# Kernel optimization log

Measured on AMD Instinct MI355X. Metric: run time of the kernel, lower is better.

The kernel has to match this reference:

```python
import jax, jax.numpy as jnp
import numpy as np
from jax import lax

NUM_CLASSES = 80
BOX_GAIN, CLS_GAIN, OBJ_GAIN = 7.5, 0.5, 1.0
LABEL_SMOOTH = 0.0
BATCH, NUM_T, IMG = 16, 256, 640
EPS = 1e-7


def setup_inputs() -> dict:
    key = jax.random.key(0)
    ks = jax.random.split(key, 10)
    inp = {}
    for i, g in enumerate([80, 40, 20]):
        inp[f"cls_p{i}"] = jax.random.normal(ks[i], (BATCH, NUM_CLASSES, g, g), jnp.float32)
        inp[f"reg_p{i}"] = jax.random.normal(ks[3 + i], (BATCH, 4, g, g), jnp.float32) * 0.5
    cxy = jax.random.uniform(ks[6], (NUM_T, 2), minval=32.0, maxval=float(IMG - 32))
    wh = jax.random.uniform(ks[7], (NUM_T, 2), minval=8.0, maxval=128.0)
    inp["tboxes"] = jnp.concatenate([cxy - wh / 2, cxy + wh / 2], axis=-1)  # [T,4] xyxy px
    inp["t_batch"] = jax.random.randint(ks[8], (NUM_T,), 0, BATCH, jnp.int32)
    inp["t_cls"] = jax.random.randint(ks[9], (NUM_T,), 0, NUM_CLASSES, jnp.int32)
    return inp


def _bce(z, t):
    # BCEWithLogits: softplus(z) - z*t, numerically stable
    return jnp.logaddexp(0.0, z) - z * t


def _box_iou(a, b):
    # a: [B,A,4] xyxy, b: [T,4] xyxy -> [B,A,T]
    lt = jnp.maximum(a[:, :, None, :2], b[None, None, :, :2])
    rb = jnp.minimum(a[:, :, None, 2:], b[None, None, :, 2:])
    wh = jnp.clip(rb - lt, 0.0)
    inter = wh[..., 0] * wh[..., 1]
    area_a = (a[..., 2] - a[..., 0]) * (a[..., 3] - a[..., 1])
    area_b = (b[:, 2] - b[:, 0]) * (b[:, 3] - b[:, 1])
    return inter / (area_a[:, :, None] + area_b[None, None, :] - inter + EPS)


def _ciou(p, g):
    # elementwise CIoU between matched boxes, p/g: [B,A,4] xyxy -> [B,A]
    pw, ph = p[..., 2] - p[..., 0], p[..., 3] - p[..., 1]
    gw, gh = g[..., 2] - g[..., 0], g[..., 3] - g[..., 1]
    lt = jnp.maximum(p[..., :2], g[..., :2])
    rb = jnp.minimum(p[..., 2:], g[..., 2:])
    wh = jnp.clip(rb - lt, 0.0)
    inter = wh[..., 0] * wh[..., 1]
    union = pw * ph + gw * gh - inter + EPS
    iou = inter / union
    clt = jnp.minimum(p[..., :2], g[..., :2])
    crb = jnp.maximum(p[..., 2:], g[..., 2:])
    c = crb - clt
    c2 = c[..., 0] ** 2 + c[..., 1] ** 2 + EPS  # enclosing diag^2
    pc = (p[..., :2] + p[..., 2:]) * 0.5
    gc = (g[..., :2] + g[..., 2:]) * 0.5
    rho2 = jnp.sum((pc - gc) ** 2, axis=-1)  # center dist^2
    v = (4.0 / jnp.pi ** 2) * (jnp.arctan(gw / (gh + EPS)) - jnp.arctan(pw / (ph + EPS))) ** 2
    alpha = lax.stop_gradient(v / (v - iou + 1.0 + EPS))
    return iou - rho2 / c2 - alpha * v


def _scale_loss(cls_p, reg_p, tboxes, t_batch, t_cls, stride):
    B, C, H, W = cls_p.shape
    A = H * W
    cls_p = cls_p.reshape(B, C, A).transpose(0, 2, 1)  # [B,A,C]
    reg_p = reg_p.reshape(B, 4, A).transpose(0, 2, 1)  # [B,A,4]
    gy, gx = jnp.meshgrid(jnp.arange(H, dtype=jnp.float32), jnp.arange(W, dtype=jnp.float32), indexing="ij")
    grid = jnp.stack([gx, gy], axis=-1).reshape(A, 2)  # [A,2] (x,y), row-major over (h,w)
    # decode: xy = (sigmoid + grid)*stride, wh = exp*stride -> xyxy
    xy = (jax.nn.sigmoid(reg_p[..., :2]) + grid) * stride
    wh = jnp.exp(reg_p[..., 2:4]) * stride
    boxes = jnp.concatenate([xy - wh * 0.5, xy + wh * 0.5], axis=-1)  # [B,A,4]
    # pairwise IoU vs all targets, mask targets from other images
    iou = _box_iou(boxes, tboxes)  # [B,A,T]
    valid = t_batch[None, None, :] == jnp.arange(B, dtype=t_batch.dtype)[:, None, None]
    iou = jnp.where(valid, iou, -1.0)
    max_iou = jnp.max(iou, axis=-1)
    best = jnp.argmax(iou, axis=-1)  # [B,A]
    pos = max_iou > 0.5  # positive anchor mask
    npos = jnp.maximum(jnp.sum(pos), 1)
    # box loss: (1 - CIoU) averaged over positives
    mt_boxes = tboxes[best]  # [B,A,4] gathered matched GT
    ciou = _ciou(boxes, mt_boxes)
    box_loss = jnp.sum(jnp.where(pos, 1.0 - ciou, 0.0)) / npos
    # cls loss: BCE with (smoothed) one-hot over positive anchors
    cp, cn = 1.0 - 0.5 * LABEL_SMOOTH, 0.5 * LABEL_SMOOTH
    cls_t = jax.nn.one_hot(t_cls[best], C, dtype=cls_p.dtype) * (cp - cn) + cn
    cls_loss = jnp.sum(_bce(cls_p, cls_t) * pos[..., None]) / (npos * C)
    # obj loss: BCE of max class logit vs positivity, over all anchors
    obj_logit = jnp.max(cls_p, axis=-1)
    obj_loss = jnp.mean(_bce(obj_logit, pos.astype(cls_p.dtype)))
    return BOX_GAIN * box_loss + CLS_GAIN * cls_loss + OBJ_GAIN * obj_loss


def reference(cls_p0, cls_p1, cls_p2, reg_p0, reg_p1, reg_p2, tboxes, t_batch, t_cls):
    total = jnp.float32(0.0)
    for i, (c, r) in enumerate([(cls_p0, reg_p0), (cls_p1, reg_p1), (cls_p2, reg_p2)]):
        total = total + _scale_loss(c, r, tboxes, t_batch, t_cls, float(8 * 2 ** i))
    return total
```

## Files before the change

### kernel.cpp

```cpp
#include <hip/hip_runtime.h>
#include <math.h>

#define C_NUM 80
#define T_NUM 256
#define EPSF  1e-7f
#define NBLK  2112

__device__ __forceinline__ float softplusf(float z) {
    return fmaxf(z, 0.0f) + log1pf(expf(-fabsf(z)));
}

typedef float vfloat4 __attribute__((ext_vector_type(4)));
__device__ __forceinline__ float4 ldnt4(const float* p) {
    vfloat4 v = __builtin_nontemporal_load(reinterpret_cast<const vfloat4*>(p));
    return make_float4(v.x, v.y, v.z, v.w);
}
__device__ __forceinline__ float ldnt(const float* p) {
    return __builtin_nontemporal_load(p);
}

__global__ __launch_bounds__(256)
void yolo_main(const float* __restrict__ cls0, const float* __restrict__ cls1,
               const float* __restrict__ cls2,
               const float* __restrict__ reg0, const float* __restrict__ reg1,
               const float* __restrict__ reg2,
               const float* __restrict__ tboxes, const int* __restrict__ t_batch,
               const int* __restrict__ t_cls, float4* __restrict__ pblk)
{
    __shared__ float s_x1[T_NUM], s_y1[T_NUM], s_x2[T_NUM], s_y2[T_NUM], s_ar[T_NUM];
    __shared__ int   s_tc[T_NUM];
    __shared__ int   s_list[T_NUM];
    __shared__ int   s_wcnt[4];
    __shared__ float4 s_wmax4[256];
    __shared__ int   s_btc[64] __attribute__((aligned(16)));
    __shared__ float s_red[4][4];

    const int tid = threadIdx.x;
    const int bid = blockIdx.x;
    const int lane = tid & 63, wave = tid >> 6;
    const int cq = lane >> 4, ag = lane & 15;

    int b, a0, A, H; float stride;
    const float *clsp, *regp;
    if (bid < 1600)      { b = bid / 100;            a0 = (bid % 100) * 64; A = 6400; H = 80; stride =  8.f; clsp = cls0; regp = reg0; }
    else if (bid < 2000) { int r = bid - 1600; b = r / 25; a0 = (r % 25) * 64; A = 1600; H = 40; stride = 16.f; clsp = cls1; regp = reg1; }
    else                 { int r = bid - 2000; b = r / 7;  a0 = (r % 7)  * 64; A = 400;  H = 20; stride = 32.f; clsp = cls2; regp = reg2; }

    const int cbase = wave * 20 + cq * 5;
    const int ga = a0 + 4 * ag;
    const float* p = clsp + ((size_t)(b * C_NUM + cbase)) * (size_t)A + ((ga < A) ? ga : a0);
    float4 z0 = ldnt4(p);
    float4 z1 = ldnt4(p + (size_t)A);
    float4 z2 = ldnt4(p + 2 * (size_t)A);
    float4 z3 = ldnt4(p + 3 * (size_t)A);
    float4 z4 = ldnt4(p + 4 * (size_t)A);

    const int am = a0 + lane;
    const bool amv = am < A;
    float rx = 0.f, ry = 0.f, rw = 0.f, rh = 0.f;
    {
        const float* rp = regp + (size_t)(b * 4) * (size_t)A + (amv ? am : 0);
        if (wave == 0) { rx = ldnt(rp); ry = ldnt(rp + A); rw = ldnt(rp + 2 * (size_t)A); rh = ldnt(rp + 3 * (size_t)A); }
    }

    {
        float4 t4 = reinterpret_cast<const float4*>(tboxes)[tid];
        s_x1[tid] = t4.x; s_y1[tid] = t4.y; s_x2[tid] = t4.z; s_y2[tid] = t4.w;
        s_ar[tid] = (t4.z - t4.x) * (t4.w - t4.y);
        s_tc[tid] = t_cls[tid];
    }
    int match = (t_batch[tid] == b) ? 1 : 0;
    unsigned long long mask = __ballot(match != 0);
    if (lane == 0) s_wcnt[wave] = __popcll(mask);
    if (match) {
        int pfx = __popcll(mask & (((unsigned long long)1 << lane) - 1ull));
        s_list[wave * 64 + pfx] = tid;
    }
    __syncthreads();

    float cnt = 0.f, boxs = 0.f;
    if (wave == 0) {
        if (amv) {
            float gx = (float)(am % H), gy = (float)(am / H);
            float x = (1.f / (1.f + expf(-rx)) + gx) * stride;
            float y = (1.f / (1.f + expf(-ry)) + gy) * stride;
            float w = expf(rw) * stride;
            float h = expf(rh) * stride;
            float px1 = x - 0.5f * w, py1 = y - 0.5f * h;
            float px2 = x + 0.5f * w, py2 = y + 0.5f * h;
            float pw = px2 - px1, ph = py2 - py1;
            float parea = pw * ph;

            float maxiou = -1.f; int best = 0;
            #pragma unroll
            for (int w4 = 0; w4 < 4; ++w4) {
                const int cw = s_wcnt[w4];
                for (int j = 0; j < cw; ++j) {
                    int t = s_list[w4 * 64 + j];
                    float ix = fminf(px2, s_x2[t]) - fmaxf(px1, s_x1[t]);
                    float iy = fminf(py2, s_y2[t]) - fmaxf(py1, s_y1[t]);
                    float inter = fmaxf(ix, 0.f) * fmaxf(iy, 0.f);
                    float iou = inter / (parea + s_ar[t] - inter + EPSF);
                    if (iou > maxiou) { maxiou = iou; best = t; }
                }
            }
            const bool pos = maxiou > 0.5f;
            s_btc[lane] = pos ? s_tc[best] : -1;

            if (pos) {
                cnt = 1.f;
                float gx1 = s_x1[best], gy1 = s_y1[best], gx2 = s_x2[best], gy2 = s_y2[best];
                float gw = gx2 - gx1, gh = gy2 - gy1;
                float ix = fminf(px2, gx2) - fmaxf(px1, gx1);
                float iy = fminf(py2, gy2) - fmaxf(py1, gy1);
                float inter = fmaxf(ix, 0.f) * fmaxf(iy, 0.f);
                float uni = parea + gw * gh - inter + EPSF;
                float iou = inter / uni;
                float cw = fmaxf(px2, gx2) - fminf(px1, gx1);
                float ch = fmaxf(py2, gy2) - fminf(py1, gy1);
                float c2 = cw * cw + ch * ch + EPSF;
                float dx = 0.5f * ((px1 + px2) - (gx1 + gx2));
                float dy = 0.5f * ((py1 + py2) - (gy1 + gy2));
                float rho2 = dx * dx + dy * dy;
                float dv = atanf(gw / (gh + EPSF)) - atanf(pw / (ph + EPSF));
                float v = 0.40528473456935108577f * dv * dv;
                float alpha = v / (v - iou + 1.f + EPSF);
                boxs = 1.f - (iou - rho2 / c2 - alpha * v);
            }
        } else {
            s_btc[lane] = -1;
        }
    }

    {
        float4 mx;
        mx.x = fmaxf(fmaxf(fmaxf(z0.x, z1.x), fmaxf(z2.x, z3.x)), z4.x);
        mx.y = fmaxf(fmaxf(fmaxf(z0.y, z1.y), fmaxf(z2.y, z3.y)), z4.y);
        mx.z = fmaxf(fmaxf(fmaxf(z0.z, z1.z), fmaxf(z2.z, z3.z)), z4.z);
        mx.w = fmaxf(fmaxf(fmaxf(z0.w, z1.w), fmaxf(z2.w, z3.w)), z4.w);
        s_wmax4[tid] = mx;
    }
    __syncthreads();

    float clss = 0.f;
    bool lanepos;
    {
        int4 t4 = *reinterpret_cast<const int4*>(&s_btc[4 * ag]);
        lanepos = (t4.x >= 0) | (t4.y >= 0) | (t4.z >= 0) | (t4.w >= 0);
        if (lanepos) {
            const float4 zz[5] = { z0, z1, z2, z3, z4 };
            #pragma unroll
            for (int k = 0; k < 5; ++k) {
                const int cg = cbase + k;
                if (t4.x >= 0) { clss += softplusf(zz[k].x); if (cg == t4.x) clss -= zz[k].x; }
                if (t4.y >= 0) { clss += softplusf(zz[k].y); if (cg == t4.y) clss -= zz[k].y; }
                if (t4.z >= 0) { clss += softplusf(zz[k].z); if (cg == t4.z) clss -= zz[k].z; }
                if (t4.w >= 0) { clss += softplusf(zz[k].w); if (cg == t4.w) clss -= zz[k].w; }
            }
        }
    }

    float objs = 0.f;
    if (wave == 0 && amv) {
        const float* wm = reinterpret_cast<const float*>(s_wmax4);
        float m = -INFINITY;
        #pragma unroll
        for (int wq = 0; wq < 16; ++wq)
            m = fmaxf(m, wm[wq * 64 + lane]);
        bool pos = s_btc[lane] >= 0;
        objs = softplusf(m) - (pos ? m : 0.f);
    }

    unsigned long long bp = __ballot(lanepos);
    if (bp) {
        #pragma unroll
        for (int off = 32; off > 0; off >>= 1)
            clss += __shfl_down(clss, off, 64);
    }
    if (lane == 0) s_red[wave][2] = clss;
    if (wave == 0) {
        #pragma unroll
        for (int off = 32; off > 0; off >>= 1) {
            cnt  += __shfl_down(cnt,  off, 64);
            boxs += __shfl_down(boxs, off, 64);
            objs += __shfl_down(objs, off, 64);
        }
        if (lane == 0) { s_red[0][0] = cnt; s_red[0][1] = boxs; s_red[0][3] = objs; }
    }
    __syncthreads();
    if (tid == 0) {
        float4 v;
        v.x = s_red[0][0];
        v.y = s_red[0][1];
        v.z = s_red[0][2] + s_red[1][2] + s_red[2][2] + s_red[3][2];
        v.w = s_red[0][3];
        pblk[bid] = v;
    }
}

__global__ __launch_bounds__(256)
void yolo_finalize(const float4* __restrict__ pblk, float* __restrict__ out)
{
    __shared__ float s_red[4][12];
    const int tid = threadIdx.x, lane = tid & 63, wave = tid >> 6;

    float v[12];
    #pragma unroll
    for (int j = 0; j < 12; ++j) v[j] = 0.f;
    for (int i = tid; i < NBLK; i += 256) {
        float4 q = pblk[i];
        int k = (i < 1600) ? 0 : (i < 2000) ? 4 : 8;
        v[k + 0] += q.x; v[k + 1] += q.y; v[k + 2] += q.z; v[k + 3] += q.w;
    }
    #pragma unroll
    for (int off = 32; off > 0; off >>= 1) {
        #pragma unroll
        for (int j = 0; j < 12; ++j) v[j] += __shfl_down(v[j], off, 64);
    }
    if (lane == 0) {
        #pragma unroll
        for (int j = 0; j < 12; ++j) s_red[wave][j] = v[j];
    }
    __syncthreads();
    if (tid == 0) {
        float t[12];
        #pragma unroll
        for (int j = 0; j < 12; ++j)
            t[j] = s_red[0][j] + s_red[1][j] + s_red[2][j] + s_red[3][j];
        const float inv_anch[3] = { 1.f / (16.f * 6400.f), 1.f / (16.f * 1600.f), 1.f / (16.f * 400.f) };
        float total = 0.f;
        #pragma unroll
        for (int k = 0; k < 3; ++k) {
            float np = fmaxf(t[k * 4 + 0], 1.f);
            total += 7.5f * t[k * 4 + 1] / np
                   + 0.5f * t[k * 4 + 2] / (np * (float)C_NUM)
                   + t[k * 4 + 3] * inv_anch[k];
        }
        out[0] = total;
    }
}

extern "C" void kernel_launch(void* const* d_in, const int* in_sizes, int n_in,
                              void* d_out, int out_size, void* d_ws, size_t ws_size,
                              hipStream_t stream) {
    const float *cls[3] = {nullptr, nullptr, nullptr};
    const float *reg[3] = {nullptr, nullptr, nullptr};
    const float *tboxes = nullptr;
    const int *t_batch = nullptr, *t_cls = nullptr;
    for (int i = 0; i < n_in; ++i) {
        switch (in_sizes[i]) {
            case 16 * 80 * 6400: cls[0] = (const float*)d_in[i]; break;
            case 16 * 80 * 1600: cls[1] = (const float*)d_in[i]; break;
            case 16 * 80 * 400:  cls[2] = (const float*)d_in[i]; break;
            case 16 * 4 * 6400:  reg[0] = (const float*)d_in[i]; break;
            case 16 * 4 * 1600:  reg[1] = (const float*)d_in[i]; break;
            case 16 * 4 * 400:   reg[2] = (const float*)d_in[i]; break;
            case 256 * 4:        tboxes = (const float*)d_in[i]; break;
            case 256:
                if (!t_batch) t_batch = (const int*)d_in[i];
                else          t_cls   = (const int*)d_in[i];
                break;
            default: break;
        }
    }
    float4* pblk = (float4*)d_ws;
    float*  out  = (float*)d_out;

    hipLaunchKernelGGL(yolo_main, dim3(NBLK), dim3(256), 0, stream,
                       cls[0], cls[1], cls[2], reg[0], reg[1], reg[2],
                       tboxes, t_batch, t_cls, pblk);
    hipLaunchKernelGGL(yolo_finalize, dim3(1), dim3(256), 0, stream, pblk, out);
}
```

Before: 111.8 us.

## Process 128 anchors per block with two matching waves and plain loads

Each block now handles 128 anchors instead of 64, halving the block count. Two waves do the IoU matching and CIoU work, and each thread loads two float4 groups per class row. The per-block prologue of staging targets and building the match list is amortized over twice as many anchors. Nontemporal loads are replaced with ordinary loads, and the target and regression loads are hoisted ahead of the class loads. Having fewer blocks may reduce occupancy and latency hiding on the memory-bound class read, and each thread now uses more registers.

Result: faster. 106.4 us, median of 2 (-4.8%).

```diff
diff --git a/kernel.cpp b/kernel.cpp
--- a/kernel.cpp
+++ b/kernel.cpp
@@ -4,19 +4,10 @@
 #define C_NUM 80
 #define T_NUM 256
 #define EPSF  1e-7f
-#define NBLK  2112
+#define NBLK  1072
 
 __device__ __forceinline__ float softplusf(float z) {
     return fmaxf(z, 0.0f) + log1pf(expf(-fabsf(z)));
-}
-
-typedef float vfloat4 __attribute__((ext_vector_type(4)));
-__device__ __forceinline__ float4 ldnt4(const float* p) {
-    vfloat4 v = __builtin_nontemporal_load(reinterpret_cast<const vfloat4*>(p));
-    return make_float4(v.x, v.y, v.z, v.w);
-}
-__device__ __forceinline__ float ldnt(const float* p) {
-    return __builtin_nontemporal_load(p);
 }
 
 __global__ __launch_bounds__(256)
@@ -31,8 +22,8 @@
     __shared__ int   s_tc[T_NUM];
     __shared__ int   s_list[T_NUM];
     __shared__ int   s_wcnt[4];
-    __shared__ float4 s_wmax4[256];
-    __shared__ int   s_btc[64] __attribute__((aligned(16)));
+    __shared__ float4 s_wmax4[2][256];
+    __shared__ int   s_btc[128] __attribute__((aligned(16)));
     __shared__ float s_red[4][4];
 
     const int tid = threadIdx.x;
@@ -42,34 +33,43 @@
 
     int b, a0, A, H; float stride;
     const float *clsp, *regp;
-    if (bid < 1600)      { b = bid / 100;            a0 = (bid % 100) * 64; A = 6400; H = 80; stride =  8.f; clsp = cls0; regp = reg0; }
-    else if (bid < 2000) { int r = bid - 1600; b = r / 25; a0 = (r % 25) * 64; A = 1600; H = 40; stride = 16.f; clsp = cls1; regp = reg1; }
-    else                 { int r = bid - 2000; b = r / 7;  a0 = (r % 7)  * 64; A = 400;  H = 20; stride = 32.f; clsp = cls2; regp = reg2; }
+    if (bid < 800)       { b = bid / 50;            a0 = (bid % 50) * 128; A = 6400; H = 80; stride =  8.f; clsp = cls0; regp = reg0; }
+    else if (bid < 1008) { int r = bid - 800;  b = r / 13; a0 = (r % 13) * 128; A = 1600; H = 40; stride = 16.f; clsp = cls1; regp = reg1; }
+    else                 { int r = bid - 1008; b = r / 4;  a0 = (r % 4)  * 128; A = 400;  H = 20; stride = 32.f; clsp = cls2; regp = reg2; }
+
+    float4 t4 = reinterpret_cast<const float4*>(tboxes)[tid];
+    int    tb = t_batch[tid];
+    int    tc = t_cls[tid];
+
+    const int am = a0 + (wave << 6) + lane;
+    const bool amv = (wave < 2) && (am < A);
+    float rx = 0.f, ry = 0.f, rw = 0.f, rh = 0.f;
+    if (wave < 2) {
+        const float* rp = regp + (size_t)(b * 4) * (size_t)A + (amv ? am : a0);
+        rx = rp[0]; ry = rp[A]; rw = rp[2 * (size_t)A]; rh = rp[3 * (size_t)A];
+    }
 
     const int cbase = wave * 20 + cq * 5;
-    const int ga = a0 + 4 * ag;
-    const float* p = clsp + ((size_t)(b * C_NUM + cbase)) * (size_t)A + ((ga < A) ? ga : a0);
-    float4 z0 = ldnt4(p);
-    float4 z1 = ldnt4(p + (size_t)A);
-    float4 z2 = ldnt4(p + 2 * (size_t)A);
-    float4 z3 = ldnt4(p + 3 * (size_t)A);
-    float4 z4 = ldnt4(p + 4 * (size_t)A);
-
-    const int am = a0 + lane;
-    const bool amv = am < A;
-    float rx = 0.f, ry = 0.f, rw = 0.f, rh = 0.f;
-    {
-        const float* rp = regp + (size_t)(b * 4) * (size_t)A + (amv ? am : 0);
-        if (wave == 0) { rx = ldnt(rp); ry = ldnt(rp + A); rw = ldnt(rp + 2 * (size_t)A); rh = ldnt(rp + 3 * (size_t)A); }
-    }
-
-    {
-        float4 t4 = reinterpret_cast<const float4*>(tboxes)[tid];
-        s_x1[tid] = t4.x; s_y1[tid] = t4.y; s_x2[tid] = t4.z; s_y2[tid] = t4.w;
-        s_ar[tid] = (t4.z - t4.x) * (t4.w - t4.y);
-        s_tc[tid] = t_cls[tid];
-    }
-    int match = (t_batch[tid] == b) ? 1 : 0;
+    const int ga0 = a0 + 4 * ag;
+    const int ga1 = a0 + 64 + 4 * ag;
+    const float* pc = clsp + ((size_t)(b * C_NUM + cbase)) * (size_t)A;
+    const float* p0 = pc + ((ga0 < A) ? ga0 : a0);
+    const float* p1 = pc + ((ga1 < A) ? ga1 : a0);
+    float4 za0 = *reinterpret_cast<const float4*>(p0);
+    float4 za1 = *reinterpret_cast<const float4*>(p0 + (size_t)A);
+    float4 za2 = *reinterpret_cast<const float4*>(p0 + 2 * (size_t)A);
+    float4 za3 = *reinterpret_cast<const float4*>(p0 + 3 * (size_t)A);
+    float4 za4 = *reinterpret_cast<const float4*>(p0 + 4 * (size_t)A);
+    float4 zb0 = *reinterpret_cast<const float4*>(p1);
+    float4 zb1 = *reinterpret_cast<const float4*>(p1 + (size_t)A);
+    float4 zb2 = *reinterpret_cast<const float4*>(p1 + 2 * (size_t)A);
+    float4 zb3 = *reinterpret_cast<const float4*>(p1 + 3 * (size_t)A);
+    float4 zb4 = *reinterpret_cast<const float4*>(p1 + 4 * (size_t)A);
+
+    s_x1[tid] = t4.x; s_y1[tid] = t4.y; s_x2[tid] = t4.z; s_y2[tid] = t4.w;
+    s_ar[tid] = (t4.z - t4.x) * (t4.w - t4.y);
+    s_tc[tid] = tc;
+    int match = (tb == b) ? 1 : 0;
     unsigned long long mask = __ballot(match != 0);
     if (lane == 0) s_wcnt[wave] = __popcll(mask);
     if (match) {
@@ -79,7 +79,8 @@
     __syncthreads();
 
     float cnt = 0.f, boxs = 0.f;
-    if (wave == 0) {
+    if (wave < 2) {
+        const int slot = (wave << 6) + lane;
         if (amv) {
             float gx = (float)(am % H), gy = (float)(am / H);
             float x = (1.f / (1.f + expf(-rx)) + gx) * stride;
@@ -105,7 +106,7 @@
                 }
             }
             const bool pos = maxiou > 0.5f;
-            s_btc[lane] = pos ? s_tc[best] : -1;
+            s_btc[slot] = pos ? s_tc[best] : -1;
 
             if (pos) {
                 cnt = 1.f;
@@ -128,46 +129,65 @@
                 boxs = 1.f - (iou - rho2 / c2 - alpha * v);
             }
         } else {
-            s_btc[lane] = -1;
+            s_btc[slot] = -1;
         }
     }
 
     {
         float4 mx;
-        mx.x = fmaxf(fmaxf(fmaxf(z0.x, z1.x), fmaxf(z2.x, z3.x)), z4.x);
-        mx.y = fmaxf(fmaxf(fmaxf(z0.y, z1.y), fmaxf(z2.y, z3.y)), z4.y);
-        mx.z = fmaxf(fmaxf(fmaxf(z0.z, z1.z), fmaxf(z2.z, z3.z)), z4.z);
-        mx.w = fmaxf(fmaxf(fmaxf(z0.w, z1.w), fmaxf(z2.w, z3.w)), z4.w);
-        s_wmax4[tid] = mx;
+        mx.x = fmaxf(fmaxf(fmaxf(za0.x, za1.x), fmaxf(za2.x, za3.x)), za4.x);
+        mx.y = fmaxf(fmaxf(fmaxf(za0.y, za1.y), fmaxf(za2.y, za3.y)), za4.y);
+        mx.z = fmaxf(fmaxf(fmaxf(za0.z, za1.z), fmaxf(za2.z, za3.z)), za4.z);
+        mx.w = fmaxf(fmaxf(fmaxf(za0.w, za1.w), fmaxf(za2.w, za3.w)), za4.w);
+        s_wmax4[0][tid] = mx;
+        mx.x = fmaxf(fmaxf(fmaxf(zb0.x, zb1.x), fmaxf(zb2.x, zb3.x)), zb4.x);
+        mx.y = fmaxf(fmaxf(fmaxf(zb0.y, zb1.y), fmaxf(zb2.y, zb3.y)), zb4.y);
+        mx.z = fmaxf(fmaxf(fmaxf(zb0.z, zb1.z), fmaxf(zb2.z, zb3.z)), zb4.z);
+        mx.w = fmaxf(fmaxf(fmaxf(zb0.w, zb1.w), fmaxf(zb2.w, zb3.w)), zb4.w);
+        s_wmax4[1][tid] = mx;
     }
     __syncthreads();
 
     float clss = 0.f;
     bool lanepos;
     {
-        int4 t4 = *reinterpret_cast<const int4*>(&s_btc[4 * ag]);
-        lanepos = (t4.x >= 0) | (t4.y >= 0) | (t4.z >= 0) | (t4.w >= 0);
-        if (lanepos) {
-            const float4 zz[5] = { z0, z1, z2, z3, z4 };
+        int4 ta = *reinterpret_cast<const int4*>(&s_btc[4 * ag]);
+        int4 tb4 = *reinterpret_cast<const int4*>(&s_btc[64 + 4 * ag]);
+        bool pa = (ta.x >= 0) | (ta.y >= 0) | (ta.z >= 0) | (ta.w >= 0);
+        bool pb = (tb4.x >= 0) | (tb4.y >= 0) | (tb4.z >= 0) | (tb4.w >= 0);
+        lanepos = pa | pb;
+        if (pa) {
+            const float4 zz[5] = { za0, za1, za2, za3, za4 };
             #pragma unroll
             for (int k = 0; k < 5; ++k) {
                 const int cg = cbase + k;
-                if (t4.x >= 0) { clss += softplusf(zz[k].x); if (cg == t4.x) clss -= zz[k].x; }
-                if (t4.y >= 0) { clss += softplusf(zz[k].y); if (cg == t4.y) clss -= zz[k].y; }
-                if (t4.z >= 0) { clss += softplusf(zz[k].z); if (cg == t4.z) clss -= zz[k].z; }
-                if (t4.w >= 0) { clss += softplusf(zz[k].w); if (cg == t4.w) clss -= zz[k].w; }
+                if (ta.x >= 0) { clss += softplusf(zz[k].x); if (cg == ta.x) clss -= zz[k].x; }
+                if (ta.y >= 0) { clss += softplusf(zz[k].y); if (cg == ta.y) clss -= zz[k].y; }
+                if (ta.z >= 0) { clss += softplusf(zz[k].z); if (cg == ta.z) clss -= zz[k].z; }
+                if (ta.w >= 0) { clss += softplusf(zz[k].w); if (cg == ta.w) clss -= zz[k].w; }
+            }
+        }
+        if (pb) {
+            const float4 zz[5] = { zb0, zb1, zb2, zb3, zb4 };
+            #pragma unroll
+            for (int k = 0; k < 5; ++k) {
+                const int cg = cbase + k;
+                if (tb4.x >= 0) { clss += softplusf(zz[k].x); if (cg == tb4.x) clss -= zz[k].x; }
+                if (tb4.y >= 0) { clss += softplusf(zz[k].y); if (cg == tb4.y) clss -= zz[k].y; }
+                if (tb4.z >= 0) { clss += softplusf(zz[k].z); if (cg == tb4.z) clss -= zz[k].z; }
+                if (tb4.w >= 0) { clss += softplusf(zz[k].w); if (cg == tb4.w) clss -= zz[k].w; }
             }
         }
     }
 
     float objs = 0.f;
-    if (wave == 0 && amv) {
-        const float* wm = reinterpret_cast<const float*>(s_wmax4);
+    if (wave < 2 && amv) {
+        const float* wm = reinterpret_cast<const float*>(s_wmax4[wave]);
         float m = -INFINITY;
         #pragma unroll
         for (int wq = 0; wq < 16; ++wq)
             m = fmaxf(m, wm[wq * 64 + lane]);
-        bool pos = s_btc[lane] >= 0;
+        bool pos = s_btc[(wave << 6) + lane] >= 0;
         objs = softplusf(m) - (pos ? m : 0.f);
     }
 
@@ -178,22 +198,22 @@
             clss += __shfl_down(clss, off, 64);
     }
     if (lane == 0) s_red[wave][2] = clss;
-    if (wave == 0) {
+    if (wave < 2) {
         #pragma unroll
         for (int off = 32; off > 0; off >>= 1) {
             cnt  += __shfl_down(cnt,  off, 64);
             boxs += __shfl_down(boxs, off, 64);
             objs += __shfl_down(objs, off, 64);
         }
-        if (lane == 0) { s_red[0][0] = cnt; s_red[0][1] = boxs; s_red[0][3] = objs; }
+        if (lane == 0) { s_red[wave][0] = cnt; s_red[wave][1] = boxs; s_red[wave][3] = objs; }
     }
     __syncthreads();
     if (tid == 0) {
         float4 v;
-        v.x = s_red[0][0];
-        v.y = s_red[0][1];
+        v.x = s_red[0][0] + s_red[1][0];
+        v.y = s_red[0][1] + s_red[1][1];
         v.z = s_red[0][2] + s_red[1][2] + s_red[2][2] + s_red[3][2];
-        v.w = s_red[0][3];
+        v.w = s_red[0][3] + s_red[1][3];
         pblk[bid] = v;
     }
 }
@@ -209,7 +229,7 @@
     for (int j = 0; j < 12; ++j) v[j] = 0.f;
     for (int i = tid; i < NBLK; i += 256) {
         float4 q = pblk[i];
-        int k = (i < 1600) ? 0 : (i < 2000) ? 4 : 8;
+        int k = (i < 800) ? 0 : (i < 1008) ? 4 : 8;
         v[k + 0] += q.x; v[k + 1] += q.y; v[k + 2] += q.z; v[k + 3] += q.w;
     }
     #pragma unroll
```
